# Optimization experiments

Measured on AMD Instinct MI355X. Metric: run time of the kernel, lower is better.

## Reference

```python
import jax, jax.numpy as jnp
import numpy as np
from jax import lax

HID = 128      # GNN hidden dim (node_label_embedding_size)
EMB = 64       # char-CNN output (graph_node_label_representation_size)
N_LAYERS = 6
N_ETYPES = 12
CHAR_EMB = 16
KW = 5         # conv kernel width
LEAKY = 0.2


def _gru(x, h, k, rk, b):
    # keras-style GRU cell: gates z, r, candidate hh; new h = z*h + (1-z)*hh
    H = h.shape[-1]
    g = x @ k + b                       # [N, 3H]
    z = jax.nn.sigmoid(g[:, :H] + h @ rk[:, :H])
    r = jax.nn.sigmoid(g[:, H:2 * H] + h @ rk[:, H:2 * H])
    hh = jnp.tanh(g[:, 2 * H:] + (r * h) @ rk[:, 2 * H:])
    return z * h + (1.0 - z) * hh


def setup_inputs() -> dict:
    key = jax.random.key(0)
    ks = jax.random.split(key, 32)
    N, U, L, E, G = 100000, 20000, 16, 100000, 64
    inp = {}
    inp["graphs_in_batch"] = G
    inp["node_labels_unique"] = jax.random.randint(ks[0], (U, L), 0, 256, dtype=jnp.int32)
    inp["node_labels_index"] = jax.random.randint(ks[1], (N,), 0, U, dtype=jnp.int32)
    inp["node_to_graph"] = jnp.sort(jax.random.randint(ks[2], (N,), 0, G, dtype=jnp.int32))
    inp["regression_labels"] = jax.random.normal(ks[3], (G,), dtype=jnp.float32)
    for t in range(N_ETYPES):
        inp[f"adj_{t}"] = jax.random.randint(ks[4 + t], (E, 2), 0, N, dtype=jnp.int32)
    # learned params
    inp["char_embed"] = jax.random.normal(ks[16], (256, CHAR_EMB), dtype=jnp.float32) * 0.1
    inp["conv_w"] = jax.random.normal(ks[17], (KW, CHAR_EMB, EMB), dtype=jnp.float32) / np.sqrt(KW * CHAR_EMB)
    inp["conv_b"] = jnp.zeros((EMB,), dtype=jnp.float32)
    inp["W_msg"] = jax.random.normal(ks[18], (N_LAYERS, N_ETYPES, HID, HID), dtype=jnp.float32) / np.sqrt(HID)
    inp["gru_k"] = jax.random.normal(ks[19], (N_LAYERS, HID, 3 * HID), dtype=jnp.float32) / np.sqrt(HID)
    inp["gru_rk"] = jax.random.normal(ks[20], (N_LAYERS, HID, 3 * HID), dtype=jnp.float32) / np.sqrt(HID)
    inp["gru_b"] = jnp.zeros((N_LAYERS, 3 * HID), dtype=jnp.float32)
    inp["score_w"] = jax.random.normal(ks[21], (HID, 1), dtype=jnp.float32) / np.sqrt(HID)
    inp["score_b"] = jnp.zeros((1,), dtype=jnp.float32)
    inp["mlp_w1"] = jax.random.normal(ks[22], (HID, 128), dtype=jnp.float32) / np.sqrt(HID)
    inp["mlp_b1"] = jnp.zeros((128,), dtype=jnp.float32)
    inp["mlp_w2"] = jax.random.normal(ks[23], (128, 32), dtype=jnp.float32) / np.sqrt(128)
    inp["mlp_b2"] = jnp.zeros((32,), dtype=jnp.float32)
    inp["mlp_w3"] = jax.random.normal(ks[24], (32, 8), dtype=jnp.float32) / np.sqrt(32)
    inp["mlp_b3"] = jnp.zeros((8,), dtype=jnp.float32)
    inp["mlp_w4"] = jax.random.normal(ks[25], (8, 1), dtype=jnp.float32) / np.sqrt(8)
    inp["mlp_b4"] = jnp.zeros((1,), dtype=jnp.float32)
    return inp


def reference(graphs_in_batch, node_labels_unique, node_labels_index, node_to_graph,
              regression_labels, adj_0, adj_1, adj_2, adj_3, adj_4, adj_5, adj_6,
              adj_7, adj_8, adj_9, adj_10, adj_11, char_embed, conv_w, conv_b,
              W_msg, gru_k, gru_rk, gru_b, score_w, score_b,
              mlp_w1, mlp_b1, mlp_w2, mlp_b2, mlp_w3, mlp_b3, mlp_w4, mlp_b4):
    adj = jnp.stack([adj_0, adj_1, adj_2, adj_3, adj_4, adj_5, adj_6,
                     adj_7, adj_8, adj_9, adj_10, adj_11])  # [T, E, 2]
    # --- char-CNN node label embedding ---
    chars = char_embed[node_labels_unique]                  # [U, L, CE]
    conv = lax.conv_general_dilated(chars, conv_w, (1,), 'SAME',
                                    dimension_numbers=('NWC', 'WIO', 'NWC'))
    label_rep = jnp.max(jax.nn.relu(conv + conv_b), axis=1)  # [U, EMB]
    feats = label_rep[node_labels_index]                     # [N, EMB]
    N = feats.shape[0]
    # pad initial features up to hidden_dim
    h = jnp.pad(feats, ((0, 0), (0, HID - EMB)))             # [N, HID]
    src = adj[:, :, 0]                                       # [T, E]
    tgt = adj[:, :, 1].reshape(-1)                           # [T*E]
    # --- 6-layer GGNN message passing ---
    for layer in range(N_LAYERS):
        h_src = h[src]                                       # [T, E, HID]
        msgs = jnp.einsum('teh,thd->ted', h_src, W_msg[layer])
        agg = jax.ops.segment_sum(msgs.reshape(-1, HID), tgt, num_segments=N)
        h = _gru(agg, h, gru_k[layer], gru_rk[layer], gru_b[layer])
    # --- weighted-sum graph readout (sigmoid weights, leaky_relu MLP) ---
    scores = jax.nn.sigmoid(h @ score_w + score_b)           # [N, 1]
    v = jax.nn.leaky_relu(h @ mlp_w1 + mlp_b1, LEAKY)
    v = jax.nn.leaky_relu(v @ mlp_w2 + mlp_b2, LEAKY)
    v = jax.nn.leaky_relu(v @ mlp_w3 + mlp_b3, LEAKY)
    v = v @ mlp_w4 + mlp_b4                                  # [N, 1]
    graph_rep = jax.ops.segment_sum(scores * v, node_to_graph,
                                    num_segments=graphs_in_batch)  # [G, 1]
    return graph_rep
```

## Files before the change

### kernel.cpp

```cpp
#include <hip/hip_runtime.h>
#include <hip/hip_bf16.h>

#define LEAKY_SLOPE 0.2f

typedef short short8 __attribute__((ext_vector_type(8)));
typedef short short4v __attribute__((ext_vector_type(4)));
typedef float f32x4 __attribute__((ext_vector_type(4)));

static inline int cdiv(int a, int b) { return (a + b - 1) / b; }

__device__ __forceinline__ float bf2f(unsigned short s) {
    return __uint_as_float(((unsigned int)s) << 16);
}
__device__ __forceinline__ unsigned short f2bf(float x) {
    unsigned int u = __float_as_uint(x);
    return (unsigned short)((u + 0x7FFFu + ((u >> 16) & 1u)) >> 16);
}
__device__ __forceinline__ unsigned short bf_hi(float x, float& rem) {
    unsigned int u = __float_as_uint(x);
    unsigned int hi = (u + 0x7FFFu + ((u >> 16) & 1u)) & 0xFFFF0000u;
    rem = x - __uint_as_float(hi);
    return (unsigned short)(hi >> 16);
}

struct EdgeArgs {
    const int* adj[12];
    int E[12];
    int colOff[12];
};

__global__ __launch_bounds__(64) void label_kernel(
    const int* __restrict__ labels, const float* __restrict__ char_embed,
    const float* __restrict__ conv_w, const float* __restrict__ conv_b,
    float* __restrict__ lr, int U)
{
    __shared__ float ch[20][16];
    __shared__ int lab[16];
    const int u = blockIdx.x, t = threadIdx.x;
    {
        const int r = t >> 4, i = t & 15;
        const int padrow[4] = {0, 1, 18, 19};
        ch[padrow[r]][i] = 0.f;
    }
    if (t < 16) lab[t] = labels[(size_t)u * 16 + t];
    float cwr[5][16];
    #pragma unroll
    for (int k = 0; k < 5; ++k)
        #pragma unroll
        for (int i = 0; i < 16; ++i)
            cwr[k][i] = conv_w[(k * 16 + i) * 64 + t];
    __syncthreads();
    for (int j = t; j < 256; j += 64)
        ch[2 + (j >> 4)][j & 15] = char_embed[(size_t)lab[j >> 4] * 16 + (j & 15)];
    __syncthreads();
    float aw[16];
    const float b = conv_b[t];
    #pragma unroll
    for (int w = 0; w < 16; ++w) aw[w] = b;
    #pragma unroll
    for (int x = 0; x < 20; ++x)
        #pragma unroll
        for (int i = 0; i < 16; ++i) {
            const float chv = ch[x][i];
            #pragma unroll
            for (int k = 0; k < 5; ++k) {
                const int w = x - k;
                if (w >= 0 && w < 16) aw[w] += chv * cwr[k][i];
            }
        }
    float m = 0.f;
    #pragma unroll
    for (int w = 0; w < 16; ++w) m = fmaxf(m, aw[w]);
    lr[(size_t)u * 64 + t] = m;
}

__global__ void init_h_split(const int* __restrict__ idx, const float* __restrict__ lr,
                             unsigned short* __restrict__ hS, int N, int NP)
{
    const int i = blockIdx.x * blockDim.x + threadIdx.x;
    if (i >= NP * 16) return;
    const int n = i >> 4, kg = i & 15;
    const size_t u = (size_t)(n >> 7) * 32768 + (size_t)kg * 1024 + (size_t)(n & 127) * 8;
    short8 hi, lo;
    if (n < N && kg < 8) {
        const int id = idx[n];
        #pragma unroll
        for (int j = 0; j < 8; ++j) {
            const float v = lr[(size_t)id * 64 + kg * 8 + j];
            float r; hi[j] = (short)bf_hi(v, r); lo[j] = (short)f2bf(r);
        }
    } else {
        #pragma unroll
        for (int j = 0; j < 8; ++j) { hi[j] = 0; lo[j] = 0; }
    }
    *(short8*)(hS + u) = hi;
    *(short8*)(hS + u + 16384) = lo;
}

__global__ void hist_kernel(EdgeArgs ea, int* __restrict__ deg, int N)
{
    const int t = blockIdx.y;
    const int e = blockIdx.x * blockDim.x + threadIdx.x;
    if (e >= ea.E[t]) return;
    atomicAdd(&deg[(size_t)t * N + ea.adj[t][2 * e + 1]], 1);
}

__global__ __launch_bounds__(256) void scan_a(const int* __restrict__ deg,
                                              int* __restrict__ partial, int N, int nchunk)
{
    const int t = blockIdx.y, b = blockIdx.x;
    const int base = b * 2048;
    int s = 0;
    for (int i = threadIdx.x; i < 2048; i += 256) {
        const int g = base + i;
        if (g < N) s += deg[(size_t)t * N + g];
    }
    __shared__ int sm[256];
    sm[threadIdx.x] = s; __syncthreads();
    for (int off = 128; off > 0; off >>= 1) {
        if (threadIdx.x < off) sm[threadIdx.x] += sm[threadIdx.x + off];
        __syncthreads();
    }
    if (threadIdx.x == 0) partial[t * nchunk + b] = sm[0];
}

__global__ void scan_b(int* __restrict__ partial, int nchunk)
{
    const int t = threadIdx.x;
    if (t >= 12) return;
    int off = 0;
    for (int i = 0; i < nchunk; ++i) {
        const int s = partial[t * nchunk + i];
        partial[t * nchunk + i] = off;
        off += s;
    }
}

__global__ __launch_bounds__(256) void scan_c(const int* __restrict__ deg,
                                              const int* __restrict__ partial,
                                              int* __restrict__ rowptr, int N, int nchunk)
{
    const int t = blockIdx.y, b = blockIdx.x;
    int* rp = rowptr + (size_t)t * (N + 1);
    const int base = b * 2048;
    int v[8]; int s = 0;
    #pragma unroll
    for (int j = 0; j < 8; ++j) {
        const int g = base + threadIdx.x * 8 + j;
        v[j] = (g < N) ? deg[(size_t)t * N + g] : 0;
        s += v[j];
    }
    __shared__ int ts[256];
    ts[threadIdx.x] = s; __syncthreads();
    for (int off = 1; off < 256; off <<= 1) {
        const int val = (threadIdx.x >= off) ? ts[threadIdx.x - off] : 0;
        __syncthreads();
        ts[threadIdx.x] += val;
        __syncthreads();
    }
    int run = partial[t * nchunk + b] + (threadIdx.x ? ts[threadIdx.x - 1] : 0);
    #pragma unroll
    for (int j = 0; j < 8; ++j) {
        const int g = base + threadIdx.x * 8 + j;
        run += v[j];
        if (g < N) rp[g + 1] = run;
    }
    if (b == 0 && threadIdx.x == 0) rp[0] = 0;
}

__global__ void fill_kernel(EdgeArgs ea, const int* __restrict__ rowptr,
                            int* __restrict__ cursor, int* __restrict__ col, int N)
{
    const int t = blockIdx.y;
    const int e = blockIdx.x * blockDim.x + threadIdx.x;
    if (e >= ea.E[t]) return;
    const int s  = ea.adj[t][2 * e];
    const int tg = ea.adj[t][2 * e + 1];
    const int pos = rowptr[(size_t)t * (N + 1) + tg] + atomicAdd(&cursor[(size_t)t * N + tg], 1);
    col[ea.colOff[t] + pos] = s;
}

struct WSrc { const float* wmsg; const float* gk; const float* grk; const float* w1; };

__global__ void split_w_kernel(WSrc s, unsigned short* __restrict__ wb, int nmat)
{
    const int gidx = blockIdx.x * 256 + threadIdx.x;
    const int m = gidx >> 14, e = gidx & 16383;
    if (m >= nmat) return;
    const int kg = e >> 10, rem = e & 1023, c = rem >> 3, j = rem & 7;
    const int k = kg * 8 + j;
    float x;
    if (m < 72) x = s.wmsg[(size_t)m * 16384 + (size_t)k * 128 + c];
    else if (m < 108) {
        const int g = m - 72, layer = g / 6, r2 = g % 6;
        const float* base = (r2 < 3) ? s.gk : s.grk;
        const int slice = r2 % 3;
        x = base[(size_t)layer * 49152 + (size_t)k * 384 + slice * 128 + c];
    } else x = s.w1[(size_t)k * 128 + c];
    float r; const unsigned short hi = bf_hi(x, r);
    wb[(size_t)m * 32768 + e] = hi;
    wb[(size_t)m * 32768 + 16384 + e] = f2bf(r);
}

__device__ __forceinline__ void stage_panel(const unsigned short* __restrict__ g,
                                            unsigned short* __restrict__ lds, int tid)
{
    #pragma unroll
    for (int i = 0; i < 16; ++i) {
        const int uo = i * 2048 + tid * 8;
        *(short8*)(lds + uo) = *(const short8*)(g + uo);
    }
}

template<int NM>
__device__ __forceinline__ void mfma_pass(const unsigned short* __restrict__ lds,
                                          const unsigned short* const* Bs,
                                          f32x4 (&acc)[NM][4][4],
                                          int wr, int wc, int lrow, int lkg)
{
    #pragma unroll 1
    for (int c = 0; c < 4; ++c) {
        const int kg = c * 4 + lkg;
        short8 ah[4], al[4];
        #pragma unroll
        for (int m = 0; m < 4; ++m) {
            const int u = kg * 1024 + (wr * 64 + m * 16 + lrow) * 8;
            ah[m] = *(const short8*)(lds + u);
            al[m] = *(const short8*)(lds + u + 16384);
        }
        #pragma unroll
        for (int t = 0; t < NM; ++t) {
            const unsigned short* __restrict__ B = Bs[t];
            short8 bh[4], bl[4];
            #pragma unroll
            for (int n = 0; n < 4; ++n) {
                const int u = kg * 1024 + (wc * 64 + n * 16 + lrow) * 8;
                bh[n] = *(const short8*)(B + u);
                bl[n] = *(const short8*)(B + u + 16384);
            }
            #pragma unroll
            for (int m = 0; m < 4; ++m)
                #pragma unroll
                for (int n = 0; n < 4; ++n) {
                    acc[t][m][n] = __builtin_amdgcn_mfma_f32_16x16x32_bf16(ah[m], bh[n], acc[t][m][n], 0, 0, 0);
                    acc[t][m][n] = __builtin_amdgcn_mfma_f32_16x16x32_bf16(ah[m], bl[n], acc[t][m][n], 0, 0, 0);
                    acc[t][m][n] = __builtin_amdgcn_mfma_f32_16x16x32_bf16(al[m], bh[n], acc[t][m][n], 0, 0, 0);
                }
        }
    }
}

template<int NM>
__global__ __launch_bounds__(256) void msg_kernel(
    const unsigned short* __restrict__ hS,
    const unsigned short* __restrict__ B0, const unsigned short* __restrict__ B1,
    float* __restrict__ out0, float* __restrict__ out1)
{
    __shared__ unsigned short lds[32768];
    const int tid = threadIdx.x;
    stage_panel(hS + (size_t)blockIdx.x * 32768, lds, tid);
    const int wave = tid >> 6, lane = tid & 63;
    const int wr = wave >> 1, wc = wave & 1, lrow = lane & 15, lkg = lane >> 4;
    f32x4 acc[NM][4][4] = {};
    __syncthreads();
    const unsigned short* Bs[2] = {B0, B1};
    mfma_pass<NM>(lds, Bs, acc, wr, wc, lrow, lkg);
    const size_t rowBase = (size_t)blockIdx.x * 128;
    #pragma unroll
    for (int t = 0; t < NM; ++t) {
        float* __restrict__ op = t ? out1 : out0;
        #pragma unroll
        for (int m = 0; m < 4; ++m)
            #pragma unroll
            for (int n = 0; n < 4; ++n) {
                const int col = wc * 64 + n * 16 + lrow;
                #pragma unroll
                for (int i = 0; i < 4; ++i) {
                    const size_t r = rowBase + wr * 64 + m * 16 + lkg * 4 + i;
                    op[r * 128 + col] = acc[t][m][n][i];
                }
            }
    }
}

__global__ __launch_bounds__(256) void zr_kernel(
    const unsigned short* __restrict__ aT, const unsigned short* __restrict__ hS,
    const unsigned short* __restrict__ k0, const unsigned short* __restrict__ k1,
    const unsigned short* __restrict__ rk0, const unsigned short* __restrict__ rk1,
    const float* __restrict__ bias,
    float* __restrict__ zOut, unsigned short* __restrict__ rhS)
{
    __shared__ unsigned short lds[32768];
    const int tid = threadIdx.x;
    const size_t pbase = (size_t)blockIdx.x * 32768;
    const int wave = tid >> 6, lane = tid & 63;
    const int wr = wave >> 1, wc = wave & 1, lrow = lane & 15, lkg = lane >> 4;
    f32x4 acc[2][4][4] = {};

    stage_panel(aT + pbase, lds, tid);
    __syncthreads();
    { const unsigned short* Bs[2] = {k0, k1};  mfma_pass<2>(lds, Bs, acc, wr, wc, lrow, lkg); }
    __syncthreads();
    stage_panel(hS + pbase, lds, tid);
    __syncthreads();
    { const unsigned short* Bs[2] = {rk0, rk1}; mfma_pass<2>(lds, Bs, acc, wr, wc, lrow, lkg); }

    const size_t rowBase = (size_t)blockIdx.x * 128;
    #pragma unroll
    for (int m = 0; m < 4; ++m)
        #pragma unroll
        for (int n = 0; n < 4; ++n) {
            const int col = wc * 64 + n * 16 + lrow;
            #pragma unroll
            for (int i = 0; i < 4; ++i) {
                const int rl = wr * 64 + m * 16 + lkg * 4 + i;
                const float z = 1.f / (1.f + __expf(-(acc[0][m][n][i] + bias[col])));
                zOut[(rowBase + rl) * 128 + col] = z;
                const float v = 1.f / (1.f + __expf(-(acc[1][m][n][i] + bias[128 + col])));
                const int hu = (col >> 3) * 1024 + rl * 8 + (col & 7);
                const float hval = bf2f(lds[hu]) + bf2f(lds[hu + 16384]);
                const float rh = v * hval;
                float rem; const unsigned short hi = bf_hi(rh, rem);
                rhS[pbase + hu] = hi;
                rhS[pbase + hu + 16384] = f2bf(rem);
            }
        }
}

__global__ __launch_bounds__(256) void gemm_lds(
    const unsigned short* __restrict__ A1, const unsigned short* __restrict__ B1,
    const unsigned short* __restrict__ A2, const unsigned short* __restrict__ B2,
    const float* __restrict__ bias, float* __restrict__ outF, int act)
{
    __shared__ unsigned short lds[32768];
    const int tid = threadIdx.x;
    const size_t pbase = (size_t)blockIdx.x * 32768;
    const int wave = tid >> 6, lane = tid & 63;
    const int wr = wave >> 1, wc = wave & 1, lrow = lane & 15, lkg = lane >> 4;
    f32x4 acc[1][4][4] = {};

    stage_panel(A1 + pbase, lds, tid);
    __syncthreads();
    { const unsigned short* Bs[2] = {B1, nullptr}; mfma_pass<1>(lds, Bs, acc, wr, wc, lrow, lkg); }
    if (A2) {
        __syncthreads();
        stage_panel(A2 + pbase, lds, tid);
        __syncthreads();
        const unsigned short* Bs[2] = {B2, nullptr};
        mfma_pass<1>(lds, Bs, acc, wr, wc, lrow, lkg);
    }
    const size_t rowBase = (size_t)blockIdx.x * 128;
    #pragma unroll
    for (int m = 0; m < 4; ++m)
        #pragma unroll
        for (int n = 0; n < 4; ++n) {
            const int col = wc * 64 + n * 16 + lrow;
            #pragma unroll
            for (int i = 0; i < 4; ++i) {
                const int rl = wr * 64 + m * 16 + lkg * 4 + i;
                float v = acc[0][m][n][i];
                if (bias) v += bias[col];
                if (act == 1) v = v > 0.f ? v : LEAKY_SLOPE * v;
                outF[(rowBase + rl) * 128 + col] = v;
            }
        }
}

__global__ __launch_bounds__(256) void gather_csr(
    const int* __restrict__ rowptr, const int* __restrict__ col,
    const float* __restrict__ M, float* __restrict__ agg, int N, int accum)
{
    const int i = blockIdx.x * blockDim.x + threadIdx.x;
    const int n = i >> 5, q = i & 31;
    if (n >= N) return;
    float4 acc;
    if (accum) acc = *reinterpret_cast<const float4*>(agg + (size_t)n * 128 + (q << 2));
    else       acc = make_float4(0.f, 0.f, 0.f, 0.f);
    for (int s = rowptr[n]; s < rowptr[n + 1]; ++s) {
        const float4 v = *reinterpret_cast<const float4*>(M + (size_t)col[s] * 128 + (q << 2));
        acc.x += v.x; acc.y += v.y; acc.z += v.z; acc.w += v.w;
    }
    *reinterpret_cast<float4*>(agg + (size_t)n * 128 + (q << 2)) = acc;
}

__global__ __launch_bounds__(256) void gather2_csr(
    const int* __restrict__ rp0, const int* __restrict__ c0, const float* __restrict__ M0,
    const int* __restrict__ rp1, const int* __restrict__ c1, const float* __restrict__ M1,
    float* __restrict__ agg, int N, int accum)
{
    const int i = blockIdx.x * blockDim.x + threadIdx.x;
    const int n = i >> 5, q = i & 31;
    if (n >= N) return;
    float4 acc;
    if (accum) acc = *reinterpret_cast<const float4*>(agg + (size_t)n * 128 + (q << 2));
    else       acc = make_float4(0.f, 0.f, 0.f, 0.f);
    for (int s = rp0[n]; s < rp0[n + 1]; ++s) {
        const float4 v = *reinterpret_cast<const float4*>(M0 + (size_t)c0[s] * 128 + (q << 2));
        acc.x += v.x; acc.y += v.y; acc.z += v.z; acc.w += v.w;
    }
    for (int s = rp1[n]; s < rp1[n + 1]; ++s) {
        const float4 v = *reinterpret_cast<const float4*>(M1 + (size_t)c1[s] * 128 + (q << 2));
        acc.x += v.x; acc.y += v.y; acc.z += v.z; acc.w += v.w;
    }
    *reinterpret_cast<float4*>(agg + (size_t)n * 128 + (q << 2)) = acc;
}

__global__ __launch_bounds__(256) void gather_split_csr(
    const int* __restrict__ rp, const int* __restrict__ cl, const float* __restrict__ M,
    const float* __restrict__ agg, unsigned short* __restrict__ aT, int N, int NP)
{
    const int i = blockIdx.x * blockDim.x + threadIdx.x;
    const int n = i >> 5, q = i & 31;
    if (n >= NP) return;
    float4 a = make_float4(0.f, 0.f, 0.f, 0.f);
    if (n < N) {
        a = *reinterpret_cast<const float4*>(agg + (size_t)n * 128 + (q << 2));
        for (int s = rp[n]; s < rp[n + 1]; ++s) {
            const float4 v = *reinterpret_cast<const float4*>(M + (size_t)cl[s] * 128 + (q << 2));
            a.x += v.x; a.y += v.y; a.z += v.z; a.w += v.w;
        }
    }
    const size_t u = (size_t)(n >> 7) * 32768 + (size_t)(q >> 1) * 1024
                   + (size_t)(n & 127) * 8 + (q & 1) * 4;
    const float vv[4] = {a.x, a.y, a.z, a.w};
    short4v hi, lo;
    #pragma unroll
    for (int j = 0; j < 4; ++j) {
        float r; hi[j] = (short)bf_hi(vv[j], r); lo[j] = (short)f2bf(r);
    }
    *(short4v*)(aT + u) = hi;
    *(short4v*)(aT + u + 16384) = lo;
}

__global__ void gru_ew2_split(const float* __restrict__ Z, const float* __restrict__ G,
                              unsigned short* __restrict__ hS, int N)
{
    const int i = blockIdx.x * blockDim.x + threadIdx.x;
    if (i >= N * 16) return;
    const int n = i >> 4, kg = i & 15;
    const size_t u = (size_t)(n >> 7) * 32768 + (size_t)kg * 1024 + (size_t)(n & 127) * 8;
    const short8 hi = *(const short8*)(hS + u);
    const short8 lo = *(const short8*)(hS + u + 16384);
    const size_t ro = (size_t)n * 128 + kg * 8;
    short8 nhi, nlo;
    #pragma unroll
    for (int j = 0; j < 8; ++j) {
        const float h = bf2f((unsigned short)hi[j]) + bf2f((unsigned short)lo[j]);
        const float z = Z[ro + j];
        const float hn = z * h + (1.f - z) * tanhf(G[ro + j]);
        float r; nhi[j] = (short)bf_hi(hn, r); nlo[j] = (short)f2bf(r);
    }
    *(short8*)(hS + u) = nhi;
    *(short8*)(hS + u + 16384) = nlo;
}

__global__ __launch_bounds__(256) void final_kernel(
    const unsigned short* __restrict__ hS, const float* __restrict__ V1,
    const int* __restrict__ n2g,
    const float* __restrict__ w2, const float* __restrict__ b2,
    const float* __restrict__ w3, const float* __restrict__ b3,
    const float* __restrict__ w4, const float* __restrict__ b4,
    const float* __restrict__ score_w, const float* __restrict__ score_b,
    float* __restrict__ out, int N)
{
    const int n = blockIdx.x * blockDim.x + threadIdx.x;
    const int nc = n < N ? n : N - 1;
    const int g = n2g[nc];

    float sp = score_b[0];
    #pragma unroll 4
    for (int kg = 0; kg < 16; ++kg) {
        const size_t u = (size_t)(nc >> 7) * 32768 + (size_t)kg * 1024 + (size_t)(nc & 127) * 8;
        const short8 hh = *(const short8*)(hS + u);
        const short8 hl = *(const short8*)(hS + u + 16384);
        #pragma unroll
        for (int j = 0; j < 8; ++j)
            sp += (bf2f((unsigned short)hh[j]) + bf2f((unsigned short)hl[j])) * score_w[kg * 8 + j];
    }

    float V2[32];
    #pragma unroll
    for (int j = 0; j < 32; ++j) V2[j] = b2[j];
    #pragma unroll 2
    for (int k = 0; k < 128; k += 4) {
        const float4 v1 = *reinterpret_cast<const float4*>(V1 + (size_t)nc * 128 + k);
        const float vv[4] = {v1.x, v1.y, v1.z, v1.w};
        #pragma unroll
        for (int kk = 0; kk < 4; ++kk)
            #pragma unroll
            for (int j = 0; j < 32; ++j)
                V2[j] += vv[kk] * w2[(k + kk) * 32 + j];
    }
    #pragma unroll
    for (int j = 0; j < 32; ++j) { const float x = V2[j]; V2[j] = x > 0.f ? x : LEAKY_SLOPE * x; }

    float V3[8];
    #pragma unroll
    for (int j = 0; j < 8; ++j) V3[j] = b3[j];
    #pragma unroll
    for (int k = 0; k < 32; ++k)
        #pragma unroll
        for (int j = 0; j < 8; ++j) V3[j] += V2[k] * w3[k * 8 + j];
    #pragma unroll
    for (int j = 0; j < 8; ++j) { const float x = V3[j]; V3[j] = x > 0.f ? x : LEAKY_SLOPE * x; }

    float o4 = b4[0];
    #pragma unroll
    for (int j = 0; j < 8; ++j) o4 += V3[j] * w4[j];

    const float sc = 1.f / (1.f + __expf(-sp));
    float val = (n < N) ? sc * o4 : 0.f;

    const int g0 = __shfl(g, 0, 64);
    if (__all(g == g0)) {
        #pragma unroll
        for (int d = 32; d > 0; d >>= 1) val += __shfl_xor(val, d, 64);
        if ((threadIdx.x & 63) == 0) unsafeAtomicAdd(out + g0, val);
    } else {
        if (n < N) unsafeAtomicAdd(out + g, val);
    }
}

extern "C" void kernel_launch(void* const* d_in, const int* in_sizes, int n_in,
                              void* d_out, int out_size, void* d_ws, size_t ws_size,
                              hipStream_t stream)
{
    (void)n_in;
    const int* labels   = (const int*)d_in[1];
    const int* nidx     = (const int*)d_in[2];
    const int* n2g      = (const int*)d_in[3];
    EdgeArgs ea;
    int Emax = 0, Etot = 0;
    for (int t = 0; t < 12; ++t) {
        ea.adj[t] = (const int*)d_in[5 + t];
        ea.E[t] = in_sizes[5 + t] / 2;
        ea.colOff[t] = Etot;
        Etot += ea.E[t];
        if (ea.E[t] > Emax) Emax = ea.E[t];
    }
    const float* char_embed = (const float*)d_in[17];
    const float* conv_w     = (const float*)d_in[18];
    const float* conv_b     = (const float*)d_in[19];
    const float* W_msg      = (const float*)d_in[20];
    const float* gru_k      = (const float*)d_in[21];
    const float* gru_rk     = (const float*)d_in[22];
    const float* gru_b      = (const float*)d_in[23];
    const float* score_w    = (const float*)d_in[24];
    const float* score_b    = (const float*)d_in[25];
    const float* w1 = (const float*)d_in[26];
    const float* b1 = (const float*)d_in[27];
    const float* w2 = (const float*)d_in[28];
    const float* b2 = (const float*)d_in[29];
    const float* w3 = (const float*)d_in[30];
    const float* b3 = (const float*)d_in[31];
    const float* w4 = (const float*)d_in[32];
    const float* b4 = (const float*)d_in[33];

    const int N = in_sizes[2];
    const int U = in_sizes[1] / 16;
    const int G = out_size;
    float* out = (float*)d_out;

    const int NPB = cdiv(N, 128);
    const int NP  = NPB * 128;
    const int NCHUNK = cdiv(N, 2048);
    const int NMAT = 109;

    float* ws = (float*)d_ws;
    size_t o = 0;
    float* lr   = ws + o; o += (size_t)U * 64;
    float* hSf  = ws + o; o += (size_t)NP * 128;
    float* Mf   = ws + o; o += (size_t)NP * 128;
    float* aggf = ws + o; o += (size_t)NP * 128;
    float* rhf  = ws + o; o += (size_t)NP * 128;
    float* wbf  = ws + o; o += (size_t)NMAT * 16384;
    int* rowptr = (int*)(ws + o);
    int* colarr = rowptr + (size_t)12 * (N + 1);
    const size_t total_bytes = o * sizeof(float)
        + ((size_t)12 * (N + 1) + (size_t)Etot) * sizeof(int);
    if (total_bytes > ws_size) return;

    unsigned short* hS  = (unsigned short*)hSf;
    unsigned short* aT  = (unsigned short*)Mf;
    unsigned short* rhS = (unsigned short*)rhf;
    unsigned short* wb  = (unsigned short*)wbf;

    int* deg     = (int*)Mf;
    int* cursor  = deg + (size_t)12 * N;
    int* partial = cursor + (size_t)12 * N;

    hipMemsetAsync(d_out, 0, (size_t)G * sizeof(float), stream);
    hipMemsetAsync(deg, 0, ((size_t)24 * N + 12 * NCHUNK) * sizeof(int), stream);

    {
        const dim3 ge(cdiv(Emax, 256), 12);
        const dim3 gs(NCHUNK, 12);
        hist_kernel<<<ge, 256, 0, stream>>>(ea, deg, N);
        scan_a<<<gs, 256, 0, stream>>>(deg, partial, N, NCHUNK);
        scan_b<<<1, 64, 0, stream>>>(partial, NCHUNK);
        scan_c<<<gs, 256, 0, stream>>>(deg, partial, rowptr, N, NCHUNK);
        fill_kernel<<<ge, 256, 0, stream>>>(ea, rowptr, cursor, colarr, N);
    }

    WSrc wsrc{W_msg, gru_k, gru_rk, w1};
    split_w_kernel<<<cdiv(NMAT * 16384, 256), 256, 0, stream>>>(wsrc, wb, NMAT);
    label_kernel<<<U, 64, 0, stream>>>(labels, char_embed, conv_w, conv_b, lr, U);
    init_h_split<<<cdiv(NP * 16, 256), 256, 0, stream>>>(nidx, lr, hS, N, NP);

    const int gatherBlocks = cdiv(N * 32, 256);
    const int gatherBlocksNP = cdiv(NP * 32, 256);
    const int ewBlocks = cdiv(N * 16, 256);
    auto rp  = [&](int t) { return rowptr + (size_t)t * (N + 1); };
    auto cp  = [&](int t) { return colarr + ea.colOff[t]; };
    auto wbm = [&](int m) { return wb + (size_t)m * 32768; };

    for (int layer = 0; layer < 6; ++layer) {
        const float* bl = gru_b + (size_t)layer * 384;
        const int mk = 72 + layer * 6;
        for (int p = 0; p < 5; ++p) {
            const int t0 = 2 * p, t1 = 2 * p + 1;
            msg_kernel<2><<<NPB, 256, 0, stream>>>(hS, wbm(layer * 12 + t0), wbm(layer * 12 + t1), Mf, rhf);
            gather2_csr<<<gatherBlocks, 256, 0, stream>>>(rp(t0), cp(t0), Mf,
                                                          rp(t1), cp(t1), rhf, aggf, N, p > 0);
        }
        msg_kernel<1><<<NPB, 256, 0, stream>>>(hS, wbm(layer * 12 + 10), nullptr, Mf, nullptr);
        gather_csr<<<gatherBlocks, 256, 0, stream>>>(rp(10), cp(10), Mf, aggf, N, 1);
        msg_kernel<1><<<NPB, 256, 0, stream>>>(hS, wbm(layer * 12 + 11), nullptr, rhf, nullptr);
        gather_split_csr<<<gatherBlocksNP, 256, 0, stream>>>(rp(11), cp(11), rhf, aggf, aT, N, NP);
        zr_kernel<<<NPB, 256, 0, stream>>>(aT, hS, wbm(mk + 0), wbm(mk + 1),
                                           wbm(mk + 3), wbm(mk + 4), bl, aggf, rhS);
        gemm_lds<<<NPB, 256, 0, stream>>>(aT, wbm(mk + 2), rhS, wbm(mk + 5), bl + 256, Mf, 0);
        gru_ew2_split<<<ewBlocks, 256, 0, stream>>>(aggf, Mf, hS, N);
    }
    gemm_lds<<<NPB, 256, 0, stream>>>(hS, wbm(108), nullptr, nullptr, b1, Mf, 1);
    final_kernel<<<cdiv(N, 256), 256, 0, stream>>>(hS, Mf, n2g, w2, b2, w3, b3, w4, b4,
                                                   score_w, score_b, out, N);
}
```

Measured before the change: 4.307 ms.

## Replace panel-staged GEMMs with double-buffered, swizzled LDS pipelined GEMM kernel

Replaces the msg, zr and gemm_lds kernels with one templated gemm_pipe kernel. Instead of copying the whole 64KB A panel into LDS up front, it streams it in K-quarters through a 2x8KB double buffer, with register prefetch and an XOR swizzle against bank conflicts. The smaller LDS footprint should raise occupancy and overlap global loads with MFMA work. The r*h product and its bf16 hi/lo split move out of the zr GEMM epilogue into a separate rh_panel kernel that converts the sigmoid output in place. That costs an extra launch and an extra round trip through memory, and it relies on rhS aliasing the rhf buffer.

```diff
diff --git a/kernel.cpp b/kernel.cpp
--- a/kernel.cpp
+++ b/kernel.cpp
@@ -202,41 +202,65 @@
     wb[(size_t)m * 32768 + 16384 + e] = f2bf(r);
 }
 
-__device__ __forceinline__ void stage_panel(const unsigned short* __restrict__ g,
-                                            unsigned short* __restrict__ lds, int tid)
-{
-    #pragma unroll
-    for (int i = 0; i < 16; ++i) {
-        const int uo = i * 2048 + tid * 8;
-        *(short8*)(lds + uo) = *(const short8*)(g + uo);
-    }
-}
-
-template<int NM>
-__device__ __forceinline__ void mfma_pass(const unsigned short* __restrict__ lds,
-                                          const unsigned short* const* Bs,
-                                          f32x4 (&acc)[NM][4][4],
-                                          int wr, int wc, int lrow, int lkg)
-{
-    #pragma unroll 1
-    for (int c = 0; c < 4; ++c) {
-        const int kg = c * 4 + lkg;
+template<int NM, int NST, int ACT>
+__global__ __launch_bounds__(256) void gemm_pipe(
+    const unsigned short* __restrict__ A0, const unsigned short* __restrict__ A1,
+    const unsigned short* __restrict__ B00, const unsigned short* __restrict__ B01,
+    const unsigned short* __restrict__ B10, const unsigned short* __restrict__ B11,
+    const float* __restrict__ bias,
+    float* __restrict__ out0, float* __restrict__ out1)
+{
+    __shared__ unsigned short lds[2][8192];
+    const int tid = threadIdx.x;
+    const size_t pbase = (size_t)blockIdx.x * 32768;
+    const unsigned short* Ap[2];
+    Ap[0] = A0 + pbase;
+    Ap[1] = A1 ? A1 + pbase : nullptr;
+    const unsigned short* Bp[2][2] = {{B00, B01}, {B10, B11}};
+    constexpr int S = NST * 4;
+
+    const int wave = tid >> 6, lane = tid & 63;
+    const int wr = wave >> 1, wc = wave & 1, lrow = lane & 15, lkg = lane >> 4;
+    f32x4 acc[NM][4][4] = {};
+    short8 r[4];
+
+    auto ldq = [&](int s) {
+        const unsigned short* __restrict__ A = Ap[s >> 2];
+        const int qb = (s & 3) * 4096;
+        r[0] = *(const short8*)(A + qb + tid * 8);
+        r[1] = *(const short8*)(A + qb + 2048 + tid * 8);
+        r[2] = *(const short8*)(A + 16384 + qb + tid * 8);
+        r[3] = *(const short8*)(A + 16384 + qb + 2048 + tid * 8);
+    };
+    auto stq = [&](int buf) {
+        unsigned short* L = lds[buf];
+        #pragma unroll
+        for (int j = 0; j < 4; ++j) {
+            const int d = ((j >> 1) << 12) + ((j & 1) << 11) + tid * 8;
+            const int sd = d ^ (((d >> 10) & 3) << 3);
+            *(short8*)(L + sd) = r[j];
+        }
+    };
+    auto mfma_q = [&](int buf, int s) {
+        const unsigned short* L = lds[buf];
+        const int q = s & 3;
         short8 ah[4], al[4];
         #pragma unroll
         for (int m = 0; m < 4; ++m) {
-            const int u = kg * 1024 + (wr * 64 + m * 16 + lrow) * 8;
-            ah[m] = *(const short8*)(lds + u);
-            al[m] = *(const short8*)(lds + u + 16384);
+            int u = (lkg << 10) + (wr * 64 + m * 16 + lrow) * 8;
+            u ^= (lkg << 3);
+            ah[m] = *(const short8*)(L + u);
+            al[m] = *(const short8*)(L + u + 4096);
         }
         #pragma unroll
         for (int t = 0; t < NM; ++t) {
-            const unsigned short* __restrict__ B = Bs[t];
+            const unsigned short* __restrict__ B = Bp[s >> 2][t];
             short8 bh[4], bl[4];
             #pragma unroll
             for (int n = 0; n < 4; ++n) {
-                const int u = kg * 1024 + (wc * 64 + n * 16 + lrow) * 8;
-                bh[n] = *(const short8*)(B + u);
-                bl[n] = *(const short8*)(B + u + 16384);
+                const int ub = (q * 4 + lkg) * 1024 + (wc * 64 + n * 16 + lrow) * 8;
+                bh[n] = *(const short8*)(B + ub);
+                bl[n] = *(const short8*)(B + ub + 16384);
             }
             #pragma unroll
             for (int m = 0; m < 4; ++m)
@@ -247,24 +271,21 @@
                     acc[t][m][n] = __builtin_amdgcn_mfma_f32_16x16x32_bf16(al[m], bh[n], acc[t][m][n], 0, 0, 0);
                 }
         }
-    }
-}
-
-template<int NM>
-__global__ __launch_bounds__(256) void msg_kernel(
-    const unsigned short* __restrict__ hS,
-    const unsigned short* __restrict__ B0, const unsigned short* __restrict__ B1,
-    float* __restrict__ out0, float* __restrict__ out1)
-{
-    __shared__ unsigned short lds[32768];
-    const int tid = threadIdx.x;
-    stage_panel(hS + (size_t)blockIdx.x * 32768, lds, tid);
-    const int wave = tid >> 6, lane = tid & 63;
-    const int wr = wave >> 1, wc = wave & 1, lrow = lane & 15, lkg = lane >> 4;
-    f32x4 acc[NM][4][4] = {};
+    };
+
+    ldq(0); stq(0);
+    if (S > 1) ldq(1);
     __syncthreads();
-    const unsigned short* Bs[2] = {B0, B1};
-    mfma_pass<NM>(lds, Bs, acc, wr, wc, lrow, lkg);
+    #pragma unroll
+    for (int s = 0; s < S; ++s) {
+        mfma_q(s & 1, s);
+        if (s + 1 < S) {
+            stq((s + 1) & 1);
+            if (s + 2 < S) ldq(s + 2);
+            __syncthreads();
+        }
+    }
+
     const size_t rowBase = (size_t)blockIdx.x * 128;
     #pragma unroll
     for (int t = 0; t < NM; ++t) {
@@ -276,94 +297,51 @@
                 const int col = wc * 64 + n * 16 + lrow;
                 #pragma unroll
                 for (int i = 0; i < 4; ++i) {
-                    const size_t r = rowBase + wr * 64 + m * 16 + lkg * 4 + i;
-                    op[r * 128 + col] = acc[t][m][n][i];
+                    const size_t rg = rowBase + wr * 64 + m * 16 + lkg * 4 + i;
+                    float v = acc[t][m][n][i];
+                    if (ACT != 0) v += bias[t * 128 + col];
+                    if (ACT == 1) v = v > 0.f ? v : LEAKY_SLOPE * v;
+                    else if (ACT == 2) v = 1.f / (1.f + __expf(-v));
+                    op[rg * 128 + col] = v;
                 }
             }
     }
 }
 
-__global__ __launch_bounds__(256) void zr_kernel(
-    const unsigned short* __restrict__ aT, const unsigned short* __restrict__ hS,
-    const unsigned short* __restrict__ k0, const unsigned short* __restrict__ k1,
-    const unsigned short* __restrict__ rk0, const unsigned short* __restrict__ rk1,
-    const float* __restrict__ bias,
-    float* __restrict__ zOut, unsigned short* __restrict__ rhS)
-{
-    __shared__ unsigned short lds[32768];
+__global__ __launch_bounds__(256) void rh_panel(const unsigned short* __restrict__ hS,
+                                                float* __restrict__ R)
+{
+    __shared__ float ld[16384];
     const int tid = threadIdx.x;
-    const size_t pbase = (size_t)blockIdx.x * 32768;
-    const int wave = tid >> 6, lane = tid & 63;
-    const int wr = wave >> 1, wc = wave & 1, lrow = lane & 15, lkg = lane >> 4;
-    f32x4 acc[2][4][4] = {};
-
-    stage_panel(aT + pbase, lds, tid);
+    const size_t pf = (size_t)blockIdx.x * 16384;
+    #pragma unroll
+    for (int j = 0; j < 16; ++j) {
+        const int idx = j * 1024 + tid * 4;
+        const int row = idx >> 7, col = idx & 127;
+        const float4 v = *(const float4*)(R + pf + idx);
+        *(float4*)(ld + row * 128 + (col ^ ((row & 7) << 2))) = v;
+    }
     __syncthreads();
-    { const unsigned short* Bs[2] = {k0, k1};  mfma_pass<2>(lds, Bs, acc, wr, wc, lrow, lkg); }
-    __syncthreads();
-    stage_panel(hS + pbase, lds, tid);
-    __syncthreads();
-    { const unsigned short* Bs[2] = {rk0, rk1}; mfma_pass<2>(lds, Bs, acc, wr, wc, lrow, lkg); }
-
-    const size_t rowBase = (size_t)blockIdx.x * 128;
-    #pragma unroll
-    for (int m = 0; m < 4; ++m)
-        #pragma unroll
-        for (int n = 0; n < 4; ++n) {
-            const int col = wc * 64 + n * 16 + lrow;
-            #pragma unroll
-            for (int i = 0; i < 4; ++i) {
-                const int rl = wr * 64 + m * 16 + lkg * 4 + i;
-                const float z = 1.f / (1.f + __expf(-(acc[0][m][n][i] + bias[col])));
-                zOut[(rowBase + rl) * 128 + col] = z;
-                const float v = 1.f / (1.f + __expf(-(acc[1][m][n][i] + bias[128 + col])));
-                const int hu = (col >> 3) * 1024 + rl * 8 + (col & 7);
-                const float hval = bf2f(lds[hu]) + bf2f(lds[hu + 16384]);
-                const float rh = v * hval;
-                float rem; const unsigned short hi = bf_hi(rh, rem);
-                rhS[pbase + hu] = hi;
-                rhS[pbase + hu + 16384] = f2bf(rem);
-            }
-        }
-}
-
-__global__ __launch_bounds__(256) void gemm_lds(
-    const unsigned short* __restrict__ A1, const unsigned short* __restrict__ B1,
-    const unsigned short* __restrict__ A2, const unsigned short* __restrict__ B2,
-    const float* __restrict__ bias, float* __restrict__ outF, int act)
-{
-    __shared__ unsigned short lds[32768];
-    const int tid = threadIdx.x;
-    const size_t pbase = (size_t)blockIdx.x * 32768;
-    const int wave = tid >> 6, lane = tid & 63;
-    const int wr = wave >> 1, wc = wave & 1, lrow = lane & 15, lkg = lane >> 4;
-    f32x4 acc[1][4][4] = {};
-
-    stage_panel(A1 + pbase, lds, tid);
-    __syncthreads();
-    { const unsigned short* Bs[2] = {B1, nullptr}; mfma_pass<1>(lds, Bs, acc, wr, wc, lrow, lkg); }
-    if (A2) {
-        __syncthreads();
-        stage_panel(A2 + pbase, lds, tid);
-        __syncthreads();
-        const unsigned short* Bs[2] = {B2, nullptr};
-        mfma_pass<1>(lds, Bs, acc, wr, wc, lrow, lkg);
-    }
-    const size_t rowBase = (size_t)blockIdx.x * 128;
-    #pragma unroll
-    for (int m = 0; m < 4; ++m)
-        #pragma unroll
-        for (int n = 0; n < 4; ++n) {
-            const int col = wc * 64 + n * 16 + lrow;
-            #pragma unroll
-            for (int i = 0; i < 4; ++i) {
-                const int rl = wr * 64 + m * 16 + lkg * 4 + i;
-                float v = acc[0][m][n][i];
-                if (bias) v += bias[col];
-                if (act == 1) v = v > 0.f ? v : LEAKY_SLOPE * v;
-                outF[(rowBase + rl) * 128 + col] = v;
-            }
-        }
+    unsigned short* out = (unsigned short*)(R + pf);
+    const unsigned short* hp = hS + (size_t)blockIdx.x * 32768;
+    #pragma unroll
+    for (int j = 0; j < 8; ++j) {
+        const int u = j * 2048 + tid * 8;
+        const int row = (u >> 3) & 127, kg = u >> 10;
+        const short8 hh = *(const short8*)(hp + u);
+        const short8 hl = *(const short8*)(hp + u + 16384);
+        short8 rhi, rlo;
+        #pragma unroll
+        for (int q = 0; q < 8; ++q) {
+            const int col = kg * 8 + q;
+            const float rv = ld[row * 128 + (col ^ ((row & 7) << 2))];
+            const float h = bf2f((unsigned short)hh[q]) + bf2f((unsigned short)hl[q]);
+            const float x = rv * h;
+            float rem; rhi[q] = (short)bf_hi(x, rem); rlo[q] = (short)f2bf(rem);
+        }
+        *(short8*)(out + u) = rhi;
+        *(short8*)(out + u + 16384) = rlo;
+    }
 }
 
 __global__ __launch_bounds__(256) void gather_csr(
@@ -619,20 +597,27 @@
         const int mk = 72 + layer * 6;
         for (int p = 0; p < 5; ++p) {
             const int t0 = 2 * p, t1 = 2 * p + 1;
-            msg_kernel<2><<<NPB, 256, 0, stream>>>(hS, wbm(layer * 12 + t0), wbm(layer * 12 + t1), Mf, rhf);
+            gemm_pipe<2, 1, 0><<<NPB, 256, 0, stream>>>(
+                hS, nullptr, wbm(layer * 12 + t0), wbm(layer * 12 + t1),
+                nullptr, nullptr, nullptr, Mf, rhf);
             gather2_csr<<<gatherBlocks, 256, 0, stream>>>(rp(t0), cp(t0), Mf,
                                                           rp(t1), cp(t1), rhf, aggf, N, p > 0);
         }
-        msg_kernel<1><<<NPB, 256, 0, stream>>>(hS, wbm(layer * 12 + 10), nullptr, Mf, nullptr);
+        gemm_pipe<1, 1, 0><<<NPB, 256, 0, stream>>>(
+            hS, nullptr, wbm(layer * 12 + 10), nullptr, nullptr, nullptr, nullptr, Mf, nullptr);
         gather_csr<<<gatherBlocks, 256, 0, stream>>>(rp(10), cp(10), Mf, aggf, N, 1);
-        msg_kernel<1><<<NPB, 256, 0, stream>>>(hS, wbm(layer * 12 + 11), nullptr, rhf, nullptr);
+        gemm_pipe<1, 1, 0><<<NPB, 256, 0, stream>>>(
+            hS, nullptr, wbm(layer * 12 + 11), nullptr, nullptr, nullptr, nullptr, rhf, nullptr);
         gather_split_csr<<<gatherBlocksNP, 256, 0, stream>>>(rp(11), cp(11), rhf, aggf, aT, N, NP);
-        zr_kernel<<<NPB, 256, 0, stream>>>(aT, hS, wbm(mk + 0), wbm(mk + 1),
-                                           wbm(mk + 3), wbm(mk + 4), bl, aggf, rhS);
-        gemm_lds<<<NPB, 256, 0, stream>>>(aT, wbm(mk + 2), rhS, wbm(mk + 5), bl + 256, Mf, 0);
+        gemm_pipe<2, 2, 2><<<NPB, 256, 0, stream>>>(
+            aT, hS, wbm(mk + 0), wbm(mk + 1), wbm(mk + 3), wbm(mk + 4), bl, aggf, rhf);
+        rh_panel<<<NPB, 256, 0, stream>>>(hS, rhf);
+        gemm_pipe<1, 2, 3><<<NPB, 256, 0, stream>>>(
+            aT, rhS, wbm(mk + 2), nullptr, wbm(mk + 5), nullptr, bl + 256, Mf, nullptr);
         gru_ew2_split<<<ewBlocks, 256, 0, stream>>>(aggf, Mf, hS, N);
     }
-    gemm_lds<<<NPB, 256, 0, stream>>>(hS, wbm(108), nullptr, nullptr, b1, Mf, 1);
+    gemm_pipe<1, 1, 1><<<NPB, 256, 0, stream>>>(
+        hS, nullptr, wbm(108), nullptr, nullptr, nullptr, b1, Mf, nullptr);
     final_kernel<<<cdiv(N, 256), 256, 0, stream>>>(hS, Mf, n2g, w2, b2, w3, b3, w4, b4,
                                                    score_w, score_b, out, N);
 }
```

Result: no change. 4.256 ms (-1.2%).
